# Kernel tuning notes

Measured on AMD Instinct MI355X. Metric: run time of the kernel, lower is better.

The kernel has to match this reference:

```python
import jax, jax.numpy as jnp
import numpy as np

N = 100000
D_FEAT = 256
HID = 128
EMB = 64
FANOUT = 16


def setup_inputs() -> dict:
    key = jax.random.key(0)
    k = jax.random.split(key, 7)
    s = 0.05
    features = jax.random.normal(k[0], (N, D_FEAT), dtype=jnp.float32)
    W1 = jax.random.normal(k[1], (HID, 2 * D_FEAT), dtype=jnp.float32) * s
    W2 = jax.random.normal(k[2], (HID, 2 * HID), dtype=jnp.float32) * s
    W3 = jax.random.normal(k[3], (HID, 2 * HID), dtype=jnp.float32) * s
    W4 = jax.random.normal(k[4], (EMB, 2 * HID), dtype=jnp.float32) * s
    nodes = jnp.arange(N, dtype=jnp.int32)
    neigh = jax.random.randint(k[5], (N, FANOUT), 0, N, dtype=jnp.int32)
    return {"features": features, "W1": W1, "W2": W2, "W3": W3, "W4": W4,
            "nodes": nodes, "neigh": neigh}


def _sage_layer(h, neigh, W):
    # MeanAggregator: mean of sampled neighbor features  [N, d]
    neigh_mean = jnp.mean(h[neigh], axis=1)
    # Encoder (gcn=False): relu(W @ cat([self, neigh_mean]).T) -> [N, out]
    combined = jnp.concatenate([h, neigh_mean], axis=1)  # [N, 2d]
    return jax.nn.relu(combined @ W.T)


def reference(features, W1, W2, W3, W4, nodes, neigh):
    h1 = _sage_layer(features, neigh, W1)  # [N, HID]
    h2 = _sage_layer(h1, neigh, W2)        # [N, HID]
    h3 = _sage_layer(h2, neigh, W3)        # [N, HID]
    h4 = _sage_layer(h3, neigh, W4)        # [N, EMB]
    # GraphEmbeddingModule.forward returns gSAGE4(n).t() -> [len(n), EMB]
    return h4[nodes]
```

## Files before the change

kernel.cpp:

```cpp
#include <hip/hip_runtime.h>
#include <hip/hip_bf16.h>


constexpr int N_NODES = 100000;
constexpr int FANOUT  = 16;

typedef __attribute__((ext_vector_type(8))) short short8;
typedef __attribute__((ext_vector_type(4))) float f32x4;

__device__ inline unsigned short bf16_rne(float f) {
    unsigned u = __float_as_uint(f);
    return (unsigned short)((u + 0x7fffu + ((u >> 16) & 1u)) >> 16);
}
__device__ inline float bf16_tof(unsigned short s) {
    return __uint_as_float(((unsigned)s) << 16);
}

__global__ __launch_bounds__(256)
void prep_Bck(const float* __restrict__ W, unsigned short* __restrict__ Bhi,
              unsigned short* __restrict__ Blo, int D_IN, int D_OUT)
{
    int i = blockIdx.x * 256 + threadIdx.x;
    int total = 2 * D_OUT * D_IN;
    if (i >= total) return;
    int c = i / D_IN, k = i % D_IN;
    float v = (c < D_OUT) ? W[(size_t)c * (2 * D_IN) + k]
                          : W[(size_t)(c - D_OUT) * (2 * D_IN) + D_IN + k];
    unsigned short hi = bf16_rne(v);
    Bhi[i] = hi;
    Blo[i] = bf16_rne(v - bf16_tof(hi));
}

__global__ __launch_bounds__(256, 3)
void gemm1(const float* __restrict__ hf,
           const unsigned short* __restrict__ Bhi,
           const unsigned short* __restrict__ Blo,
           float* __restrict__ gs, unsigned short* __restrict__ gn, int N)
{
    constexpr int K = 256, C = 256, DO = 128, LDA = 40, LDB = 40;
    __shared__ unsigned short Ah[64 * LDA], Al[64 * LDA];
    __shared__ unsigned short Bh[C * LDB], Bl[C * LDB];

    const int tid  = threadIdx.x;
    const int wave = tid >> 6;
    const int lane = tid & 63;
    const int ml   = lane & 15;
    const int quad = lane >> 4;
    const int node0 = blockIdx.x * 64;

    f32x4 acc[4][4];
    #pragma unroll
    for (int mi = 0; mi < 4; ++mi)
        #pragma unroll
        for (int ni = 0; ni < 4; ++ni)
            acc[mi][ni] = (f32x4){0.f, 0.f, 0.f, 0.f};

    for (int k0 = 0; k0 < K; k0 += 32) {
        #pragma unroll
        for (int t = 0; t < 2; ++t) {
            int idx = tid + t * 256;
            int row = idx >> 3, c4 = idx & 7;
            int nd = node0 + row; if (nd >= N) nd = N - 1;
            float4 v = *(const float4*)&hf[(size_t)nd * K + k0 + c4 * 4];
            float vv[4] = {v.x, v.y, v.z, v.w};
            unsigned short hi[4], lo[4];
            #pragma unroll
            for (int e = 0; e < 4; ++e) {
                hi[e] = bf16_rne(vv[e]);
                lo[e] = bf16_rne(vv[e] - bf16_tof(hi[e]));
            }
            *(uint2*)&Ah[row * LDA + c4 * 4] = *(const uint2*)hi;
            *(uint2*)&Al[row * LDA + c4 * 4] = *(const uint2*)lo;
        }
        #pragma unroll
        for (int t = 0; t < 8; ++t) {
            int idx = tid + t * 256;
            int pl  = idx >> 10;
            int rem = idx & 1023;
            int row = rem >> 2, ch = rem & 3;
            const unsigned short* src = (pl ? Blo : Bhi) + (size_t)row * K + k0 + ch * 8;
            unsigned short* dst = (pl ? Bl : Bh) + row * LDB + ch * 8;
            *(uint4*)dst = *(const uint4*)src;
        }
        __syncthreads();

        short8 afh[4], afl[4];
        #pragma unroll
        for (int mi = 0; mi < 4; ++mi) {
            int r = mi * 16 + ml;
            afh[mi] = *(const short8*)&Ah[r * LDA + quad * 8];
            afl[mi] = *(const short8*)&Al[r * LDA + quad * 8];
        }
        #pragma unroll
        for (int ni = 0; ni < 4; ++ni) {
            int c = wave * 64 + ni * 16 + ml;
            short8 bh = *(const short8*)&Bh[c * LDB + quad * 8];
            short8 bl = *(const short8*)&Bl[c * LDB + quad * 8];
            #pragma unroll
            for (int mi = 0; mi < 4; ++mi) {
                acc[mi][ni] = __builtin_amdgcn_mfma_f32_16x16x32_bf16(afl[mi], bh, acc[mi][ni], 0, 0, 0);
                acc[mi][ni] = __builtin_amdgcn_mfma_f32_16x16x32_bf16(afh[mi], bl, acc[mi][ni], 0, 0, 0);
                acc[mi][ni] = __builtin_amdgcn_mfma_f32_16x16x32_bf16(afh[mi], bh, acc[mi][ni], 0, 0, 0);
            }
        }
        __syncthreads();
    }

    #pragma unroll
    for (int mi = 0; mi < 4; ++mi)
        #pragma unroll
        for (int r = 0; r < 4; ++r) {
            int node = node0 + mi * 16 + quad * 4 + r;
            if (node >= N) continue;
            #pragma unroll
            for (int ni = 0; ni < 4; ++ni) {
                int c = wave * 64 + ni * 16 + ml;
                float v = acc[mi][ni][r];
                if (c < DO) gs[(size_t)node * DO + c] = v;
                else        gn[(size_t)node * DO + (c - DO)] = bf16_rne(v);
            }
        }
}

template<int C>
__global__ __launch_bounds__(256, 2)
void fused_layer(const float* __restrict__ gs_in,
                 const unsigned short* __restrict__ gn_in,
                 const int* __restrict__ neigh,
                 const unsigned short* __restrict__ Bhi,
                 const unsigned short* __restrict__ Blo,
                 float* __restrict__ gs_out,
                 unsigned short* __restrict__ gn_out, int N)
{
    constexpr int K = 128, DO = C / 2, NI = C / 64, LDAF = 136, LDB = 40;
    __shared__ unsigned short Afh[64 * LDAF], Afl[64 * LDAF];
    __shared__ unsigned short Bh[C * LDB], Bl[C * LDB];

    const int tid  = threadIdx.x;
    const int wave = tid >> 6;
    const int lane = tid & 63;
    const int ml   = lane & 15;
    const int quad = lane >> 4;
    const int node0 = blockIdx.x * 64;

    {
        const int row = tid >> 2;
        const int seg = tid & 3;
        int nd = node0 + row; if (nd >= N) nd = N - 1;
        const int4* nb4 = (const int4*)(neigh + (size_t)nd * FANOUT);
        int4 q0 = nb4[0], q1 = nb4[1], q2 = nb4[2], q3 = nb4[3];
        int ids[FANOUT] = {q0.x, q0.y, q0.z, q0.w, q1.x, q1.y, q1.z, q1.w,
                           q2.x, q2.y, q2.z, q2.w, q3.x, q3.y, q3.z, q3.w};
        float acc[32];
        #pragma unroll
        for (int c = 0; c < 32; ++c) acc[c] = 0.f;
        #pragma unroll
        for (int j = 0; j < FANOUT; ++j) {
            const uint4* src = (const uint4*)&gn_in[(size_t)ids[j] * 128 + seg * 32];
            #pragma unroll
            for (int t = 0; t < 4; ++t) {
                uint4 q = src[t];
                acc[t*8+0] += __uint_as_float(q.x << 16);
                acc[t*8+1] += __uint_as_float(q.x & 0xffff0000u);
                acc[t*8+2] += __uint_as_float(q.y << 16);
                acc[t*8+3] += __uint_as_float(q.y & 0xffff0000u);
                acc[t*8+4] += __uint_as_float(q.z << 16);
                acc[t*8+5] += __uint_as_float(q.z & 0xffff0000u);
                acc[t*8+6] += __uint_as_float(q.w << 16);
                acc[t*8+7] += __uint_as_float(q.w & 0xffff0000u);
            }
        }
        const float inv = 1.0f / (float)FANOUT;
        alignas(16) unsigned short th[32], tl[32];
        const float4* gsp = (const float4*)&gs_in[(size_t)nd * 128 + seg * 32];
        #pragma unroll
        for (int t = 0; t < 8; ++t) {
            float4 s = gsp[t];
            float sv[4] = {s.x, s.y, s.z, s.w};
            #pragma unroll
            for (int e = 0; e < 4; ++e) {
                float h = fmaxf(fmaf(acc[t*4+e], inv, sv[e]), 0.f);
                unsigned short hi = bf16_rne(h);
                th[t*4+e] = hi;
                tl[t*4+e] = bf16_rne(h - bf16_tof(hi));
            }
        }
        #pragma unroll
        for (int t = 0; t < 4; ++t) {
            *(uint4*)&Afh[row * LDAF + seg * 32 + t * 8] = *(const uint4*)&th[t * 8];
            *(uint4*)&Afl[row * LDAF + seg * 32 + t * 8] = *(const uint4*)&tl[t * 8];
        }
    }

    f32x4 acc[4][NI];
    #pragma unroll
    for (int mi = 0; mi < 4; ++mi)
        #pragma unroll
        for (int ni = 0; ni < NI; ++ni)
            acc[mi][ni] = (f32x4){0.f, 0.f, 0.f, 0.f};

    for (int k0 = 0; k0 < K; k0 += 32) {
        constexpr int TOT = 2 * C * 4;
        #pragma unroll
        for (int t = 0; t < TOT / 256; ++t) {
            int idx = tid + t * 256;
            int pl  = idx / (C * 4);
            int rem = idx % (C * 4);
            int row = rem >> 2, ch = rem & 3;
            const unsigned short* src = (pl ? Blo : Bhi) + (size_t)row * K + k0 + ch * 8;
            unsigned short* dst = (pl ? Bl : Bh) + row * LDB + ch * 8;
            *(uint4*)dst = *(const uint4*)src;
        }
        __syncthreads();

        short8 afh[4], afl[4];
        #pragma unroll
        for (int mi = 0; mi < 4; ++mi) {
            int r = mi * 16 + ml;
            afh[mi] = *(const short8*)&Afh[r * LDAF + k0 + quad * 8];
            afl[mi] = *(const short8*)&Afl[r * LDAF + k0 + quad * 8];
        }
        #pragma unroll
        for (int ni = 0; ni < NI; ++ni) {
            int c = wave * (16 * NI) + ni * 16 + ml;
            short8 bh = *(const short8*)&Bh[c * LDB + quad * 8];
            short8 bl = *(const short8*)&Bl[c * LDB + quad * 8];
            #pragma unroll
            for (int mi = 0; mi < 4; ++mi) {
                acc[mi][ni] = __builtin_amdgcn_mfma_f32_16x16x32_bf16(afl[mi], bh, acc[mi][ni], 0, 0, 0);
                acc[mi][ni] = __builtin_amdgcn_mfma_f32_16x16x32_bf16(afh[mi], bl, acc[mi][ni], 0, 0, 0);
                acc[mi][ni] = __builtin_amdgcn_mfma_f32_16x16x32_bf16(afh[mi], bh, acc[mi][ni], 0, 0, 0);
            }
        }
        __syncthreads();
    }

    #pragma unroll
    for (int mi = 0; mi < 4; ++mi)
        #pragma unroll
        for (int r = 0; r < 4; ++r) {
            int node = node0 + mi * 16 + quad * 4 + r;
            if (node >= N) continue;
            #pragma unroll
            for (int ni = 0; ni < NI; ++ni) {
                int c = wave * (16 * NI) + ni * 16 + ml;
                float v = acc[mi][ni][r];
                if (c < DO) gs_out[(size_t)node * DO + c] = v;
                else        gn_out[(size_t)node * DO + (c - DO)] = bf16_rne(v);
            }
        }
}

__global__ __launch_bounds__(256)
void agg_out(const float* __restrict__ gs4, const unsigned short* __restrict__ gn4,
             const int* __restrict__ neigh, const int* __restrict__ nodes,
             float* __restrict__ out, int N)
{
    const int i    = blockIdx.x * 32 + (threadIdx.x >> 3);
    const int lane = threadIdx.x & 7;
    if (i >= N) return;
    const int nd = nodes[i];
    const int4* nb4 = (const int4*)(neigh + (size_t)nd * FANOUT);
    int4 q0 = nb4[0], q1 = nb4[1], q2 = nb4[2], q3 = nb4[3];
    int ids[FANOUT] = {q0.x, q0.y, q0.z, q0.w, q1.x, q1.y, q1.z, q1.w,
                       q2.x, q2.y, q2.z, q2.w, q3.x, q3.y, q3.z, q3.w};
    float acc[8];
    #pragma unroll
    for (int c = 0; c < 8; ++c) acc[c] = 0.f;
    #pragma unroll
    for (int j = 0; j < FANOUT; ++j) {
        uint4 q = *(const uint4*)&gn4[(size_t)ids[j] * 64 + lane * 8];
        acc[0] += __uint_as_float(q.x << 16);
        acc[1] += __uint_as_float(q.x & 0xffff0000u);
        acc[2] += __uint_as_float(q.y << 16);
        acc[3] += __uint_as_float(q.y & 0xffff0000u);
        acc[4] += __uint_as_float(q.z << 16);
        acc[5] += __uint_as_float(q.z & 0xffff0000u);
        acc[6] += __uint_as_float(q.w << 16);
        acc[7] += __uint_as_float(q.w & 0xffff0000u);
    }
    const float inv = 1.0f / (float)FANOUT;
    const float* s = gs4 + (size_t)nd * 64 + lane * 8;
    float4 s0 = *(const float4*)&s[0];
    float4 s1 = *(const float4*)&s[4];
    float4 o0, o1;
    o0.x = fmaxf(fmaf(acc[0], inv, s0.x), 0.f);
    o0.y = fmaxf(fmaf(acc[1], inv, s0.y), 0.f);
    o0.z = fmaxf(fmaf(acc[2], inv, s0.z), 0.f);
    o0.w = fmaxf(fmaf(acc[3], inv, s0.w), 0.f);
    o1.x = fmaxf(fmaf(acc[4], inv, s1.x), 0.f);
    o1.y = fmaxf(fmaf(acc[5], inv, s1.y), 0.f);
    o1.z = fmaxf(fmaf(acc[6], inv, s1.z), 0.f);
    o1.w = fmaxf(fmaf(acc[7], inv, s1.w), 0.f);
    float* op = out + (size_t)i * 64 + lane * 8;
    *(float4*)&op[0] = o0;
    *(float4*)&op[4] = o1;
}

extern "C" void kernel_launch(void* const* d_in, const int* in_sizes, int n_in,
                              void* d_out, int out_size, void* d_ws, size_t ws_size,
                              hipStream_t stream)
{
    const float* features = (const float*)d_in[0];
    const float* W1       = (const float*)d_in[1];
    const float* W2       = (const float*)d_in[2];
    const float* W3       = (const float*)d_in[3];
    const float* W4       = (const float*)d_in[4];
    const int*   nodes    = (const int*)d_in[5];
    const int*   neigh    = (const int*)d_in[6];
    float*       out      = (float*)d_out;

    unsigned short* B1h = (unsigned short*)d_ws;
    unsigned short* B1l = B1h + 65536;
    unsigned short* B2h = B1l + 65536;
    unsigned short* B2l = B2h + 32768;
    unsigned short* B3h = B2l + 32768;
    unsigned short* B3l = B3h + 32768;
    unsigned short* B4h = B3l + 32768;
    unsigned short* B4l = B4h + 16384;
    float* gs = (float*)(B4l + 16384);
    unsigned short* gnA = (unsigned short*)(gs + (size_t)N_NODES * 128);
    unsigned short* gnB = gnA + (size_t)N_NODES * 128;
    float* gs4 = (float*)gnB;
    unsigned short* gn4 = gnB + (size_t)N_NODES * 128;

    prep_Bck<<<(65536 + 255) / 256, 256, 0, stream>>>(W1, B1h, B1l, 256, 128);
    prep_Bck<<<(32768 + 255) / 256, 256, 0, stream>>>(W2, B2h, B2l, 128, 128);
    prep_Bck<<<(32768 + 255) / 256, 256, 0, stream>>>(W3, B3h, B3l, 128, 128);
    prep_Bck<<<(16384 + 255) / 256, 256, 0, stream>>>(W4, B4h, B4l, 128, 64);

    const int grid = (N_NODES + 63) / 64;

    gemm1<<<grid, 256, 0, stream>>>(features, B1h, B1l, gs, gnA, N_NODES);
    fused_layer<256><<<grid, 256, 0, stream>>>(gs, gnA, neigh, B2h, B2l, gs, gnB, N_NODES);
    fused_layer<256><<<grid, 256, 0, stream>>>(gs, gnB, neigh, B3h, B3l, gs, gnA, N_NODES);
    fused_layer<128><<<grid, 256, 0, stream>>>(gs, gnA, neigh, B4h, B4l, gs4, gn4, N_NODES);
    agg_out<<<(N_NODES + 31) / 32, 256, 0, stream>>>(gs4, gn4, neigh, nodes, out, N_NODES);
}
```

Before: 510.0 us.

## Read weight fragments directly from global, stage full A tile, sort neighbor ids

The GEMM kernels no longer stage the B (weight) tiles through shared memory. Each wave loads its bf16 hi/lo weight fragments straight from global (L1/L2 cached), which removes the per-k-step LDS copies and barriers. gemm1 now converts the whole 64x256 A tile into LDS up front, and the launch-bounds occupancy hints are swapped (gemm1 to 2, fused_layer to 3) to match the new LDS footprints. Neighbor ids are sorted with a 16-element odd-even network before gathering, aiming for better memory locality, at the cost of extra ALU work and uncoalesced global B reads.

```diff
diff --git a/kernel.cpp b/kernel.cpp
--- a/kernel.cpp
+++ b/kernel.cpp
@@ -14,6 +14,18 @@
 }
 __device__ inline float bf16_tof(unsigned short s) {
     return __uint_as_float(((unsigned)s) << 16);
+}
+
+__device__ inline void sort16(int* v) {
+    #pragma unroll
+    for (int r = 0; r < 16; ++r) {
+        #pragma unroll
+        for (int i = r & 1; i + 1 < 16; i += 2) {
+            int lo = min(v[i], v[i + 1]);
+            int hi = max(v[i], v[i + 1]);
+            v[i] = lo; v[i + 1] = hi;
+        }
+    }
 }
 
 __global__ __launch_bounds__(256)
@@ -31,15 +43,14 @@
     Blo[i] = bf16_rne(v - bf16_tof(hi));
 }
 
-__global__ __launch_bounds__(256, 3)
+__global__ __launch_bounds__(256, 2)
 void gemm1(const float* __restrict__ hf,
            const unsigned short* __restrict__ Bhi,
            const unsigned short* __restrict__ Blo,
            float* __restrict__ gs, unsigned short* __restrict__ gn, int N)
 {
-    constexpr int K = 256, C = 256, DO = 128, LDA = 40, LDB = 40;
+    constexpr int K = 256, C = 256, DO = 128, LDA = 296;
     __shared__ unsigned short Ah[64 * LDA], Al[64 * LDA];
-    __shared__ unsigned short Bh[C * LDB], Bl[C * LDB];
 
     const int tid  = threadIdx.x;
     const int wave = tid >> 6;
@@ -48,6 +59,24 @@
     const int quad = lane >> 4;
     const int node0 = blockIdx.x * 64;
 
+    #pragma unroll
+    for (int t = 0; t < 16; ++t) {
+        int idx = tid + t * 256;
+        int row = idx >> 6, c4 = idx & 63;
+        int nd = node0 + row; if (nd >= N) nd = N - 1;
+        float4 v = *(const float4*)&hf[(size_t)nd * K + c4 * 4];
+        float vv[4] = {v.x, v.y, v.z, v.w};
+        unsigned short hi[4], lo[4];
+        #pragma unroll
+        for (int e = 0; e < 4; ++e) {
+            hi[e] = bf16_rne(vv[e]);
+            lo[e] = bf16_rne(vv[e] - bf16_tof(hi[e]));
+        }
+        *(uint2*)&Ah[row * LDA + c4 * 4] = *(const uint2*)hi;
+        *(uint2*)&Al[row * LDA + c4 * 4] = *(const uint2*)lo;
+    }
+    __syncthreads();
+
     f32x4 acc[4][4];
     #pragma unroll
     for (int mi = 0; mi < 4; ++mi)
@@ -56,46 +85,18 @@
             acc[mi][ni] = (f32x4){0.f, 0.f, 0.f, 0.f};
 
     for (int k0 = 0; k0 < K; k0 += 32) {
-        #pragma unroll
-        for (int t = 0; t < 2; ++t) {
-            int idx = tid + t * 256;
-            int row = idx >> 3, c4 = idx & 7;
-            int nd = node0 + row; if (nd >= N) nd = N - 1;
-            float4 v = *(const float4*)&hf[(size_t)nd * K + k0 + c4 * 4];
-            float vv[4] = {v.x, v.y, v.z, v.w};
-            unsigned short hi[4], lo[4];
-            #pragma unroll
-            for (int e = 0; e < 4; ++e) {
-                hi[e] = bf16_rne(vv[e]);
-                lo[e] = bf16_rne(vv[e] - bf16_tof(hi[e]));
-            }
-            *(uint2*)&Ah[row * LDA + c4 * 4] = *(const uint2*)hi;
-            *(uint2*)&Al[row * LDA + c4 * 4] = *(const uint2*)lo;
-        }
-        #pragma unroll
-        for (int t = 0; t < 8; ++t) {
-            int idx = tid + t * 256;
-            int pl  = idx >> 10;
-            int rem = idx & 1023;
-            int row = rem >> 2, ch = rem & 3;
-            const unsigned short* src = (pl ? Blo : Bhi) + (size_t)row * K + k0 + ch * 8;
-            unsigned short* dst = (pl ? Bl : Bh) + row * LDB + ch * 8;
-            *(uint4*)dst = *(const uint4*)src;
-        }
-        __syncthreads();
-
         short8 afh[4], afl[4];
         #pragma unroll
         for (int mi = 0; mi < 4; ++mi) {
             int r = mi * 16 + ml;
-            afh[mi] = *(const short8*)&Ah[r * LDA + quad * 8];
-            afl[mi] = *(const short8*)&Al[r * LDA + quad * 8];
+            afh[mi] = *(const short8*)&Ah[r * LDA + k0 + quad * 8];
+            afl[mi] = *(const short8*)&Al[r * LDA + k0 + quad * 8];
         }
         #pragma unroll
         for (int ni = 0; ni < 4; ++ni) {
             int c = wave * 64 + ni * 16 + ml;
-            short8 bh = *(const short8*)&Bh[c * LDB + quad * 8];
-            short8 bl = *(const short8*)&Bl[c * LDB + quad * 8];
+            short8 bh = *(const short8*)&Bhi[(size_t)c * K + k0 + quad * 8];
+            short8 bl = *(const short8*)&Blo[(size_t)c * K + k0 + quad * 8];
             #pragma unroll
             for (int mi = 0; mi < 4; ++mi) {
                 acc[mi][ni] = __builtin_amdgcn_mfma_f32_16x16x32_bf16(afl[mi], bh, acc[mi][ni], 0, 0, 0);
@@ -103,7 +104,6 @@
                 acc[mi][ni] = __builtin_amdgcn_mfma_f32_16x16x32_bf16(afh[mi], bh, acc[mi][ni], 0, 0, 0);
             }
         }
-        __syncthreads();
     }
 
     #pragma unroll
@@ -123,7 +123,7 @@
 }
 
 template<int C>
-__global__ __launch_bounds__(256, 2)
+__global__ __launch_bounds__(256, 3)
 void fused_layer(const float* __restrict__ gs_in,
                  const unsigned short* __restrict__ gn_in,
                  const int* __restrict__ neigh,
@@ -132,9 +132,8 @@
                  float* __restrict__ gs_out,
                  unsigned short* __restrict__ gn_out, int N)
 {
-    constexpr int K = 128, DO = C / 2, NI = C / 64, LDAF = 136, LDB = 40;
+    constexpr int K = 128, DO = C / 2, NI = C / 64, LDAF = 136;
     __shared__ unsigned short Afh[64 * LDAF], Afl[64 * LDAF];
-    __shared__ unsigned short Bh[C * LDB], Bl[C * LDB];
 
     const int tid  = threadIdx.x;
     const int wave = tid >> 6;
@@ -151,6 +150,7 @@
         int4 q0 = nb4[0], q1 = nb4[1], q2 = nb4[2], q3 = nb4[3];
         int ids[FANOUT] = {q0.x, q0.y, q0.z, q0.w, q1.x, q1.y, q1.z, q1.w,
                            q2.x, q2.y, q2.z, q2.w, q3.x, q3.y, q3.z, q3.w};
+        sort16(ids);
         float acc[32];
         #pragma unroll
         for (int c = 0; c < 32; ++c) acc[c] = 0.f;
@@ -191,6 +191,7 @@
             *(uint4*)&Afl[row * LDAF + seg * 32 + t * 8] = *(const uint4*)&tl[t * 8];
         }
     }
+    __syncthreads();
 
     f32x4 acc[4][NI];
     #pragma unroll
@@ -200,19 +201,6 @@
             acc[mi][ni] = (f32x4){0.f, 0.f, 0.f, 0.f};
 
     for (int k0 = 0; k0 < K; k0 += 32) {
-        constexpr int TOT = 2 * C * 4;
-        #pragma unroll
-        for (int t = 0; t < TOT / 256; ++t) {
-            int idx = tid + t * 256;
-            int pl  = idx / (C * 4);
-            int rem = idx % (C * 4);
-            int row = rem >> 2, ch = rem & 3;
-            const unsigned short* src = (pl ? Blo : Bhi) + (size_t)row * K + k0 + ch * 8;
-            unsigned short* dst = (pl ? Bl : Bh) + row * LDB + ch * 8;
-            *(uint4*)dst = *(const uint4*)src;
-        }
-        __syncthreads();
-
         short8 afh[4], afl[4];
         #pragma unroll
         for (int mi = 0; mi < 4; ++mi) {
@@ -223,8 +211,8 @@
         #pragma unroll
         for (int ni = 0; ni < NI; ++ni) {
             int c = wave * (16 * NI) + ni * 16 + ml;
-            short8 bh = *(const short8*)&Bh[c * LDB + quad * 8];
-            short8 bl = *(const short8*)&Bl[c * LDB + quad * 8];
+            short8 bh = *(const short8*)&Bhi[(size_t)c * K + k0 + quad * 8];
+            short8 bl = *(const short8*)&Blo[(size_t)c * K + k0 + quad * 8];
             #pragma unroll
             for (int mi = 0; mi < 4; ++mi) {
                 acc[mi][ni] = __builtin_amdgcn_mfma_f32_16x16x32_bf16(afl[mi], bh, acc[mi][ni], 0, 0, 0);
@@ -232,7 +220,6 @@
                 acc[mi][ni] = __builtin_amdgcn_mfma_f32_16x16x32_bf16(afh[mi], bh, acc[mi][ni], 0, 0, 0);
             }
         }
-        __syncthreads();
     }
 
     #pragma unroll
@@ -264,6 +251,7 @@
     int4 q0 = nb4[0], q1 = nb4[1], q2 = nb4[2], q3 = nb4[3];
     int ids[FANOUT] = {q0.x, q0.y, q0.z, q0.w, q1.x, q1.y, q1.z, q1.w,
                        q2.x, q2.y, q2.z, q2.w, q3.x, q3.y, q3.z, q3.w};
+    sort16(ids);
     float acc[8];
     #pragma unroll
     for (int c = 0; c < 8; ++c) acc[c] = 0.f;
```

Result: slower. 538.1 us (+5.5%).
